# Kernel optimization log

Hardware: AMD Instinct MI355X
Metric: run time of the kernel (lower is better)

Reference implementation:

```python
import jax, jax.numpy as jnp
import numpy as np
from jax import lax

B, S, H = 2, 2048, 768
FF = 1536
E = 8
TOP_K = 2


def setup_inputs() -> dict:
    key = jax.random.key(0)
    k1, k2, k3, k4 = jax.random.split(key, 4)
    hidden_states = jax.random.normal(k1, (B, S, H), dtype=jnp.float32)
    # torch init: weight.normal_() for experts; nn.Linear default init for gate (approx normal here is fine for a numerics baseline)
    gate_w = jax.random.normal(k2, (E, H), dtype=jnp.float32) * 0.02
    w_fc = jax.random.normal(k3, (E, FF, H), dtype=jnp.float32) * 0.02
    w_proj = jax.random.normal(k4, (E, H, FF), dtype=jnp.float32) * 0.02
    return {"hidden_states": hidden_states, "gate_w": gate_w, "w_fc": w_fc, "w_proj": w_proj}


def reference(hidden_states, gate_w, w_fc, w_proj):
    b, s, h = hidden_states.shape
    x = hidden_states.reshape(-1, h)                      # [T, H]
    # --- top-k gating (logits in float32, as in the torch code) ---
    logits = (x @ gate_w.T).astype(jnp.float32)           # [T, E]
    top_logits, top_idx = lax.top_k(logits, TOP_K)        # [T, K]
    gates = jax.nn.softmax(top_logits, axis=1).astype(x.dtype)  # [T, K]
    # combined per-token/per-expert gate: g[t,e] = sum_k gates[t,k]*[idx[t,k]==e]
    onehot = jax.nn.one_hot(top_idx, E, dtype=x.dtype)    # [T, K, E]
    g = jnp.einsum('tk,tke->te', gates, onehot)           # [T, E]
    # --- experts: gather + per-expert GEMM + gated scatter-add combine ---
    # Equivalent math: tokens with zero gate for expert e contribute nothing,
    # so compute each expert on all tokens and weight by g[:, e].
    out = jnp.zeros_like(x)
    for e in range(E):  # fixed small loop over experts (structurally distinct weights)
        hmid = jax.nn.gelu(x @ w_fc[e].T, approximate=False)   # [T, FF] (torch gelu = erf form)
        out = out + g[:, e:e + 1] * (hmid @ w_proj[e].T)       # [T, H]
    out = out.reshape(b, s, h)
    return out, logits
```

## Files before the change

kernel.cpp:

```cpp
#include <hip/hip_runtime.h>
#include <hip/hip_bf16.h>
#include <math.h>
#include <stdint.h>

#define TOKENS 4096
#define HDIM   768
#define FFDIM  1536
#define NEXP   8
#define MAXRT  72

typedef __attribute__((ext_vector_type(8))) short bf16x8;
typedef __attribute__((ext_vector_type(4))) float f32x4;

__device__ __forceinline__ unsigned short f2bf(float f) {
    union { float f; uint32_t u; } c; c.f = f;
    uint32_t u = c.u;
    uint32_t r = (u + 0x7FFFu + ((u >> 16) & 1u)) >> 16;
    return (unsigned short)r;
}

__device__ __forceinline__ void gload_lds16(const void* g, void* l) {
    __builtin_amdgcn_global_load_lds(
        (const __attribute__((address_space(1))) void*)g,
        (__attribute__((address_space(3))) void*)l, 16, 0, 0);
}

__global__ void cast_bf16_2(const float* __restrict__ s1, unsigned short* __restrict__ d1,
                            const float* __restrict__ s2, unsigned short* __restrict__ d2,
                            int n4) {
    int stride = gridDim.x * blockDim.x;
    for (int i = blockIdx.x * blockDim.x + threadIdx.x; i < 2 * n4; i += stride) {
        const float4* s = (i < n4) ? (const float4*)s1 : (const float4*)s2;
        ushort4* d = (i < n4) ? (ushort4*)d1 : (ushort4*)d2;
        int j = (i < n4) ? i : i - n4;
        float4 v = s[j];
        ushort4 o;
        o.x = f2bf(v.x); o.y = f2bf(v.y); o.z = f2bf(v.z); o.w = f2bf(v.w);
        d[j] = o;
    }
}

__global__ __launch_bounds__(256) void gating(
    const float* __restrict__ x, const float* __restrict__ gw,
    float* __restrict__ logits,
    int* __restrict__ tok_e, float* __restrict__ tok_g,
    unsigned short* __restrict__ x_bf, float* __restrict__ outp)
{
    float4 zz = make_float4(0.f, 0.f, 0.f, 0.f);
#pragma unroll
    for (int j = 0; j < 3; j++)
        ((float4*)outp)[blockIdx.x * 768 + j * 256 + threadIdx.x] = zz;

    int t = blockIdx.x * 4 + (threadIdx.x >> 6);
    int lane = threadIdx.x & 63;
    const float4* xt = (const float4*)(x + (size_t)t * HDIM);
    const float4* gw4 = (const float4*)gw;
    ushort4* xbt = (ushort4*)(x_bf + (size_t)t * HDIM);
    float acc[NEXP];
#pragma unroll
    for (int e = 0; e < NEXP; e++) acc[e] = 0.f;
#pragma unroll
    for (int it = 0; it < 3; it++) {
        int i = lane + it * 64;
        float4 xv = xt[i];
        ushort4 o;
        o.x = f2bf(xv.x); o.y = f2bf(xv.y); o.z = f2bf(xv.z); o.w = f2bf(xv.w);
        xbt[i] = o;
#pragma unroll
        for (int e = 0; e < NEXP; e++) {
            float4 wv = gw4[e * 192 + i];
            acc[e] += xv.x * wv.x + xv.y * wv.y + xv.z * wv.z + xv.w * wv.w;
        }
    }
#pragma unroll
    for (int e = 0; e < NEXP; e++) {
#pragma unroll
        for (int off = 32; off > 0; off >>= 1)
            acc[e] += __shfl_xor(acc[e], off);
    }
    if (lane == 0) {
        float4 l0 = make_float4(acc[0], acc[1], acc[2], acc[3]);
        float4 l1 = make_float4(acc[4], acc[5], acc[6], acc[7]);
        float4* lp = (float4*)(logits + (size_t)t * NEXP);
        lp[0] = l0; lp[1] = l1;
        int i0 = 0; float v0 = acc[0];
#pragma unroll
        for (int e = 1; e < NEXP; e++) if (acc[e] > v0) { v0 = acc[e]; i0 = e; }
        int i1 = -1; float v1 = -3.4e38f;
#pragma unroll
        for (int e = 0; e < NEXP; e++) if (e != i0 && acc[e] > v1) { v1 = acc[e]; i1 = e; }
        float g0 = 1.f / (1.f + expf(v1 - v0));
        tok_e[t * 2] = i0; tok_e[t * 2 + 1] = i1;
        tok_g[t * 2] = g0; tok_g[t * 2 + 1] = 1.f - g0;
    }
}

__global__ __launch_bounds__(1024) void build_lists(
    const int* __restrict__ tok_e, const float* __restrict__ tok_g,
    int* __restrict__ counts, int* __restrict__ bases,
    int* __restrict__ rtiles, int* __restrict__ nrt,
    int* __restrict__ entries, float* __restrict__ gates)
{
    __shared__ unsigned long long wlo[16], whi[16];
    int tid = threadIdx.x;
    int lane = tid & 63, wid = tid >> 6;
    int eL[8]; float gL[8];
    int4 ea = ((const int4*)tok_e)[tid * 2];
    int4 eb = ((const int4*)tok_e)[tid * 2 + 1];
    float4 ga = ((const float4*)tok_g)[tid * 2];
    float4 gb = ((const float4*)tok_g)[tid * 2 + 1];
    eL[0] = ea.x; eL[1] = ea.y; eL[2] = ea.z; eL[3] = ea.w;
    eL[4] = eb.x; eL[5] = eb.y; eL[6] = eb.z; eL[7] = eb.w;
    gL[0] = ga.x; gL[1] = ga.y; gL[2] = ga.z; gL[3] = ga.w;
    gL[4] = gb.x; gL[5] = gb.y; gL[6] = gb.z; gL[7] = gb.w;

    unsigned long long clo = 0, chi = 0;
#pragma unroll
    for (int j = 0; j < 8; j++) {
        int e = eL[j];
        unsigned long long one = 1ull << ((e & 3) * 16);
        if (e < 4) clo += one; else chi += one;
    }
    unsigned long long ilo = clo, ihi = chi;
#pragma unroll
    for (int s = 1; s < 64; s <<= 1) {
        unsigned long long t1 = __shfl_up(ilo, s);
        unsigned long long t2 = __shfl_up(ihi, s);
        if (lane >= s) { ilo += t1; ihi += t2; }
    }
    if (lane == 63) { wlo[wid] = ilo; whi[wid] = ihi; }
    __syncthreads();
    if (tid == 0) {
        unsigned long long rl = 0, rh = 0;
#pragma unroll
        for (int i = 0; i < 16; i++) {
            unsigned long long a = wlo[i], b = whi[i];
            wlo[i] = rl; whi[i] = rh;
            rl += a; rh += b;
        }
        int c[8];
#pragma unroll
        for (int e = 0; e < 4; e++) {
            c[e]     = (int)((rl >> (e * 16)) & 0xFFFF);
            c[e + 4] = (int)((rh >> (e * 16)) & 0xFFFF);
        }
        int b = 0, nt = 0;
#pragma unroll
        for (int e = 0; e < NEXP; e++) {
            counts[e] = c[e]; bases[e] = b; b += c[e];
            for (int r = 0; r < c[e]; r += 128) rtiles[nt++] = (e << 16) | r;
        }
        nrt[0] = nt;
    }
    __syncthreads();
    unsigned long long rlo = wlo[wid] + (ilo - clo);
    unsigned long long rhi = whi[wid] + (ihi - chi);
#pragma unroll
    for (int j = 0; j < 8; j++) {
        int e = eL[j];
        int sh = (e & 3) * 16;
        unsigned long long one = 1ull << sh;
        int slot;
        if (e < 4) { slot = (int)((rlo >> sh) & 0xFFFF); rlo += one; }
        else       { slot = (int)((rhi >> sh) & 0xFFFF); rhi += one; }
        entries[e * TOKENS + slot] = tid * 8 + j;
        gates[e * TOKENS + slot]   = gL[j];
    }
}

template<int KD, int ND, bool IS_FC>
__global__ __launch_bounds__(256) void moe_gemm(
    const unsigned short* __restrict__ Asrc,
    const unsigned short* __restrict__ Bsrc,
    const int* __restrict__ counts,
    const int* __restrict__ bases,
    const int* __restrict__ rtiles,
    const int* __restrict__ nrt,
    const int* __restrict__ entries,
    const float* __restrict__ gates,
    unsigned short* __restrict__ hmid,
    float* __restrict__ outp)
{
    int ti = blockIdx.y;
    if (ti >= nrt[0]) return;
    int pk   = rtiles[ti];
    int e    = pk >> 16;
    int row0 = pk & 0xFFFF;
    int n_e  = counts[e];
    int ebase = bases[e];
    int n0 = blockIdx.x * 128;

    __shared__ __align__(16) unsigned short sA[2][128 * 32];
    __shared__ __align__(16) unsigned short sB[2][128 * 32];

    int tid = threadIdx.x;
    int w = tid >> 6;
    int l = tid & 63;
    const int* lst = entries + e * TOKENS;

    int r0 = w * 32 + (l >> 2);
    int r1 = r0 + 16;
    int p  = l & 3;
    int ss0 = p ^ ((r0 >> 1) & 3);
    int ss1 = p ^ ((r1 >> 1) & 3);

    int lr0 = row0 + r0;
    int lr1 = row0 + r1;
    int id0 = lr0 < n_e ? lr0 : n_e - 1;
    int id1 = lr1 < n_e ? lr1 : n_e - 1;
    size_t arow0, arow1;
    if (IS_FC) { arow0 = (size_t)(lst[id0] >> 1); arow1 = (size_t)(lst[id1] >> 1); }
    else       { arow0 = (size_t)(ebase + id0);   arow1 = (size_t)(ebase + id1);   }

    const unsigned short* Ag0 = Asrc + arow0 * KD + ss0 * 8;
    const unsigned short* Ag1 = Asrc + arow1 * KD + ss1 * 8;
    const unsigned short* Bg0 = Bsrc + ((size_t)e * ND + n0 + r0) * KD + ss0 * 8;
    const unsigned short* Bg1 = Bsrc + ((size_t)e * ND + n0 + r1) * KD + ss1 * 8;
    int c0 = (2 * w) * 512, c1 = (2 * w + 1) * 512;

    int lo = l & 15;
    int q  = l >> 4;
    int wr = w >> 1, wc = w & 1;
    int aOff[4], bOff[4];
#pragma unroll
    for (int i = 0; i < 4; i++) {
        int m = wr * 64 + i * 16 + lo;
        aOff[i] = m * 32 + (q ^ ((m >> 1) & 3)) * 8;
        int n = wc * 64 + i * 16 + lo;
        bOff[i] = n * 32 + (q ^ ((n >> 1) & 3)) * 8;
    }

    f32x4 acc[4][4];
#pragma unroll
    for (int i = 0; i < 4; i++)
#pragma unroll
        for (int j = 0; j < 4; j++) acc[i][j] = (f32x4){0.f, 0.f, 0.f, 0.f};

    gload_lds16(Ag0, &sA[0][c0]);
    gload_lds16(Ag1, &sA[0][c1]);
    gload_lds16(Bg0, &sB[0][c0]);
    gload_lds16(Bg1, &sB[0][c1]);
    __syncthreads();

    int buf = 0;
    for (int k0 = 0; k0 < KD; k0 += 32) {
        int kn = k0 + 32;
        if (kn < KD) {
            int nb = buf ^ 1;
            gload_lds16(Ag0 + kn, &sA[nb][c0]);
            gload_lds16(Ag1 + kn, &sA[nb][c1]);
            gload_lds16(Bg0 + kn, &sB[nb][c0]);
            gload_lds16(Bg1 + kn, &sB[nb][c1]);
        }
        bf16x8 a[4], b[4];
#pragma unroll
        for (int i = 0; i < 4; i++) a[i] = *(const bf16x8*)(&sA[buf][0] + aOff[i]);
#pragma unroll
        for (int j = 0; j < 4; j++) b[j] = *(const bf16x8*)(&sB[buf][0] + bOff[j]);
#pragma unroll
        for (int i = 0; i < 4; i++)
#pragma unroll
            for (int j = 0; j < 4; j++)
                acc[i][j] = __builtin_amdgcn_mfma_f32_16x16x32_bf16(a[i], b[j], acc[i][j], 0, 0, 0);
        __syncthreads();
        buf ^= 1;
    }

#pragma unroll
    for (int i = 0; i < 4; i++) {
        int rowB = row0 + wr * 64 + i * 16 + q * 4;
#pragma unroll
        for (int rr = 0; rr < 4; rr++) {
            int orow = rowB + rr;
            if (orow < n_e) {
                if (IS_FC) {
                    size_t hrow = (size_t)(ebase + orow);
#pragma unroll
                    for (int j = 0; j < 4; j++) {
                        float v = acc[i][j][rr];
                        v = 0.5f * v * (1.f + erff(v * 0.70710678118654752f));
                        hmid[hrow * ND + n0 + wc * 64 + j * 16 + lo] = f2bf(v);
                    }
                } else {
                    int token = lst[orow] >> 1;
                    float g = gates[e * TOKENS + orow];
#pragma unroll
                    for (int j = 0; j < 4; j++) {
                        atomicAdd(&outp[(size_t)token * ND + n0 + wc * 64 + j * 16 + lo],
                                  acc[i][j][rr] * g);
                    }
                }
            }
        }
    }
}

extern "C" void kernel_launch(void* const* d_in, const int* in_sizes, int n_in,
                              void* d_out, int out_size, void* d_ws, size_t ws_size,
                              hipStream_t stream) {
    const float* x     = (const float*)d_in[0];
    const float* gw    = (const float*)d_in[1];
    const float* wfc   = (const float*)d_in[2];
    const float* wproj = (const float*)d_in[3];
    float* outp   = (float*)d_out;
    float* logits = outp + (size_t)TOKENS * HDIM;

    char* ws = (char*)d_ws;
    int*   counts  = (int*)ws;
    int*   bases   = (int*)(ws + 64);
    int*   nrt     = (int*)(ws + 128);
    int*   rtiles  = (int*)(ws + 160);
    int*   entries = (int*)(ws + 512);
    float* gates   = (float*)(ws + 512 + NEXP * TOKENS * 4);
    size_t off = 512 + 2ull * NEXP * TOKENS * 4;
    int*   tok_e   = (int*)(ws + off);   off += (size_t)TOKENS * 2 * 4;
    float* tok_g   = (float*)(ws + off); off += (size_t)TOKENS * 2 * 4;
    unsigned short* x_bf   = (unsigned short*)(ws + off); off += (size_t)TOKENS * HDIM * 2;
    unsigned short* wfc_bf = (unsigned short*)(ws + off); off += (size_t)NEXP * FFDIM * HDIM * 2;
    unsigned short* wpj_bf = (unsigned short*)(ws + off); off += (size_t)NEXP * HDIM * FFDIM * 2;
    unsigned short* hmid   = (unsigned short*)(ws + off);

    cast_bf16_2<<<2048, 256, 0, stream>>>(wfc, wfc_bf, wproj, wpj_bf,
                                          NEXP * FFDIM * HDIM / 4);
    gating<<<TOKENS / 4, 256, 0, stream>>>(x, gw, logits, tok_e, tok_g, x_bf, outp);
    build_lists<<<1, 1024, 0, stream>>>(tok_e, tok_g, counts, bases, rtiles, nrt,
                                        entries, gates);
    moe_gemm<HDIM, FFDIM, true ><<<dim3(FFDIM / 128, MAXRT), 256, 0, stream>>>(
        x_bf, wfc_bf, counts, bases, rtiles, nrt, entries, gates, hmid, outp);
    moe_gemm<FFDIM, HDIM, false><<<dim3(HDIM / 128, MAXRT), 256, 0, stream>>>(
        hmid, wpj_bf, counts, bases, rtiles, nrt, entries, gates, hmid, outp);
}
```

Measured before the change: 248.4 us.

## Use BK=64 single-buffer tiles and narrower N tile for proj GEMM

Restructures the MoE GEMM main loop from double-buffered K=32 steps to single-buffered K=64 steps with two MFMA sub-steps per barrier pair. The LDS swizzle is changed to an 8-way XOR. The N tile width becomes a template parameter, and the down-projection GEMM uses a 64-wide tile so it launches twice as many blocks. The aim is fewer barriers per unit of K and more parallelism for the smaller second GEMM. The cost is that load and compute no longer overlap within a block, and each block does less work per A-tile load in the proj GEMM.

```diff
diff --git a/kernel.cpp b/kernel.cpp
--- a/kernel.cpp
+++ b/kernel.cpp
@@ -168,7 +168,7 @@
     }
 }
 
-template<int KD, int ND, bool IS_FC>
+template<int KD, int ND, int TN, bool IS_FC>
 __global__ __launch_bounds__(256) void moe_gemm(
     const unsigned short* __restrict__ Asrc,
     const unsigned short* __restrict__ Bsrc,
@@ -181,6 +181,8 @@
     unsigned short* __restrict__ hmid,
     float* __restrict__ outp)
 {
+    constexpr int AJ = TN / 32;
+    constexpr int CB = TN / 32;
     int ti = blockIdx.y;
     if (ti >= nrt[0]) return;
     int pk   = rtiles[ti];
@@ -188,82 +190,83 @@
     int row0 = pk & 0xFFFF;
     int n_e  = counts[e];
     int ebase = bases[e];
-    int n0 = blockIdx.x * 128;
-
-    __shared__ __align__(16) unsigned short sA[2][128 * 32];
-    __shared__ __align__(16) unsigned short sB[2][128 * 32];
+    int n0 = blockIdx.x * TN;
+
+    __shared__ __align__(16) unsigned short sA[128 * 64];
+    __shared__ __align__(16) unsigned short sB[TN * 64];
 
     int tid = threadIdx.x;
     int w = tid >> 6;
     int l = tid & 63;
     const int* lst = entries + e * TOKENS;
 
-    int r0 = w * 32 + (l >> 2);
-    int r1 = r0 + 16;
-    int p  = l & 3;
-    int ss0 = p ^ ((r0 >> 1) & 3);
-    int ss1 = p ^ ((r1 >> 1) & 3);
-
-    int lr0 = row0 + r0;
-    int lr1 = row0 + r1;
-    int id0 = lr0 < n_e ? lr0 : n_e - 1;
-    int id1 = lr1 < n_e ? lr1 : n_e - 1;
-    size_t arow0, arow1;
-    if (IS_FC) { arow0 = (size_t)(lst[id0] >> 1); arow1 = (size_t)(lst[id1] >> 1); }
-    else       { arow0 = (size_t)(ebase + id0);   arow1 = (size_t)(ebase + id1);   }
-
-    const unsigned short* Ag0 = Asrc + arow0 * KD + ss0 * 8;
-    const unsigned short* Ag1 = Asrc + arow1 * KD + ss1 * 8;
-    const unsigned short* Bg0 = Bsrc + ((size_t)e * ND + n0 + r0) * KD + ss0 * 8;
-    const unsigned short* Bg1 = Bsrc + ((size_t)e * ND + n0 + r1) * KD + ss1 * 8;
-    int c0 = (2 * w) * 512, c1 = (2 * w + 1) * 512;
+    int sg = l & 7;
+    int lr8 = l >> 3;
+    const unsigned short* Ag[4];
+    int aLds[4];
+#pragma unroll
+    for (int c = 0; c < 4; c++) {
+        int rr = w * 32 + c * 8 + lr8;
+        int gr = row0 + rr;
+        int id = gr < n_e ? gr : n_e - 1;
+        size_t arow = IS_FC ? (size_t)(lst[id] >> 1) : (size_t)(ebase + id);
+        Ag[c] = Asrc + arow * KD + (size_t)((sg ^ (rr & 7)) * 8);
+        aLds[c] = (w * 32 + c * 8) * 64;
+    }
+    const unsigned short* Bg[CB];
+    int bLds[CB];
+#pragma unroll
+    for (int c = 0; c < CB; c++) {
+        int rr = w * (TN / 4) + c * 8 + lr8;
+        Bg[c] = Bsrc + ((size_t)e * ND + n0 + rr) * KD + (size_t)((sg ^ (rr & 7)) * 8);
+        bLds[c] = (w * (TN / 4) + c * 8) * 64;
+    }
 
     int lo = l & 15;
     int q  = l >> 4;
     int wr = w >> 1, wc = w & 1;
-    int aOff[4], bOff[4];
+    int aOff[4][2], bOff[AJ][2];
 #pragma unroll
     for (int i = 0; i < 4; i++) {
         int m = wr * 64 + i * 16 + lo;
-        aOff[i] = m * 32 + (q ^ ((m >> 1) & 3)) * 8;
-        int n = wc * 64 + i * 16 + lo;
-        bOff[i] = n * 32 + (q ^ ((n >> 1) & 3)) * 8;
-    }
-
-    f32x4 acc[4][4];
+#pragma unroll
+        for (int s = 0; s < 2; s++)
+            aOff[i][s] = m * 64 + ((s * 4 + q) ^ (m & 7)) * 8;
+    }
+#pragma unroll
+    for (int j = 0; j < AJ; j++) {
+        int n = wc * (TN / 2) + j * 16 + lo;
+#pragma unroll
+        for (int s = 0; s < 2; s++)
+            bOff[j][s] = n * 64 + ((s * 4 + q) ^ (n & 7)) * 8;
+    }
+
+    f32x4 acc[4][AJ];
 #pragma unroll
     for (int i = 0; i < 4; i++)
 #pragma unroll
-        for (int j = 0; j < 4; j++) acc[i][j] = (f32x4){0.f, 0.f, 0.f, 0.f};
-
-    gload_lds16(Ag0, &sA[0][c0]);
-    gload_lds16(Ag1, &sA[0][c1]);
-    gload_lds16(Bg0, &sB[0][c0]);
-    gload_lds16(Bg1, &sB[0][c1]);
-    __syncthreads();
-
-    int buf = 0;
-    for (int k0 = 0; k0 < KD; k0 += 32) {
-        int kn = k0 + 32;
-        if (kn < KD) {
-            int nb = buf ^ 1;
-            gload_lds16(Ag0 + kn, &sA[nb][c0]);
-            gload_lds16(Ag1 + kn, &sA[nb][c1]);
-            gload_lds16(Bg0 + kn, &sB[nb][c0]);
-            gload_lds16(Bg1 + kn, &sB[nb][c1]);
-        }
-        bf16x8 a[4], b[4];
-#pragma unroll
-        for (int i = 0; i < 4; i++) a[i] = *(const bf16x8*)(&sA[buf][0] + aOff[i]);
-#pragma unroll
-        for (int j = 0; j < 4; j++) b[j] = *(const bf16x8*)(&sB[buf][0] + bOff[j]);
-#pragma unroll
-        for (int i = 0; i < 4; i++)
-#pragma unroll
-            for (int j = 0; j < 4; j++)
-                acc[i][j] = __builtin_amdgcn_mfma_f32_16x16x32_bf16(a[i], b[j], acc[i][j], 0, 0, 0);
+        for (int j = 0; j < AJ; j++) acc[i][j] = (f32x4){0.f, 0.f, 0.f, 0.f};
+
+    for (int k0 = 0; k0 < KD; k0 += 64) {
+#pragma unroll
+        for (int c = 0; c < 4; c++) gload_lds16(Ag[c] + k0, sA + aLds[c]);
+#pragma unroll
+        for (int c = 0; c < CB; c++) gload_lds16(Bg[c] + k0, sB + bLds[c]);
         __syncthreads();
-        buf ^= 1;
+#pragma unroll
+        for (int s = 0; s < 2; s++) {
+            bf16x8 a[4], b[AJ];
+#pragma unroll
+            for (int i = 0; i < 4; i++) a[i] = *(const bf16x8*)(sA + aOff[i][s]);
+#pragma unroll
+            for (int j = 0; j < AJ; j++) b[j] = *(const bf16x8*)(sB + bOff[j][s]);
+#pragma unroll
+            for (int i = 0; i < 4; i++)
+#pragma unroll
+                for (int j = 0; j < AJ; j++)
+                    acc[i][j] = __builtin_amdgcn_mfma_f32_16x16x32_bf16(a[i], b[j], acc[i][j], 0, 0, 0);
+        }
+        __syncthreads();
     }
 
 #pragma unroll
@@ -276,17 +279,17 @@
                 if (IS_FC) {
                     size_t hrow = (size_t)(ebase + orow);
 #pragma unroll
-                    for (int j = 0; j < 4; j++) {
+                    for (int j = 0; j < AJ; j++) {
                         float v = acc[i][j][rr];
                         v = 0.5f * v * (1.f + erff(v * 0.70710678118654752f));
-                        hmid[hrow * ND + n0 + wc * 64 + j * 16 + lo] = f2bf(v);
+                        hmid[hrow * ND + n0 + wc * (TN / 2) + j * 16 + lo] = f2bf(v);
                     }
                 } else {
                     int token = lst[orow] >> 1;
                     float g = gates[e * TOKENS + orow];
 #pragma unroll
-                    for (int j = 0; j < 4; j++) {
-                        atomicAdd(&outp[(size_t)token * ND + n0 + wc * 64 + j * 16 + lo],
+                    for (int j = 0; j < AJ; j++) {
+                        atomicAdd(&outp[(size_t)token * ND + n0 + wc * (TN / 2) + j * 16 + lo],
                                   acc[i][j][rr] * g);
                     }
                 }
@@ -325,8 +328,8 @@
     gating<<<TOKENS / 4, 256, 0, stream>>>(x, gw, logits, tok_e, tok_g, x_bf, outp);
     build_lists<<<1, 1024, 0, stream>>>(tok_e, tok_g, counts, bases, rtiles, nrt,
                                         entries, gates);
-    moe_gemm<HDIM, FFDIM, true ><<<dim3(FFDIM / 128, MAXRT), 256, 0, stream>>>(
+    moe_gemm<HDIM, FFDIM, 128, true ><<<dim3(FFDIM / 128, MAXRT), 256, 0, stream>>>(
         x_bf, wfc_bf, counts, bases, rtiles, nrt, entries, gates, hmid, outp);
-    moe_gemm<FFDIM, HDIM, false><<<dim3(HDIM / 128, MAXRT), 256, 0, stream>>>(
+    moe_gemm<FFDIM, HDIM, 64, false><<<dim3(HDIM / 64, MAXRT), 256, 0, stream>>>(
         hmid, wpj_bf, counts, bases, rtiles, nrt, entries, gates, hmid, outp);
 }
```

Result: faster. 241.0 us (-3.0%).
